# Performance work log

Measured on AMD Instinct MI355X. Metric: run time of the kernel, lower is better.

## Reference

```python
import jax, jax.numpy as jnp
import numpy as np
from jax import lax

N, IN_CH, OUT_CH, KERNEL, D = 16, 256, 256, 3, 4096
FACTOR = 2  # upsampling factor
RESAMPLE_K = (1.0, 3.0, 3.0, 1.0)


def _fir_kernel():
    # _setup_kernel: normalize to sum 1; upsample path scales by gain * factor
    k = np.asarray(RESAMPLE_K, dtype=np.float32)
    k = k / k.sum()
    return k * FACTOR  # gain = 1


def setup_inputs() -> dict:
    key = jax.random.key(0)
    k1, k2, k3 = jax.random.split(key, 3)
    x = jax.random.normal(k1, (N, IN_CH, D), dtype=jnp.float32)
    weight = jax.random.normal(k2, (OUT_CH, IN_CH, KERNEL), dtype=jnp.float32) * 0.05
    bias = jax.random.normal(k3, (OUT_CH,), dtype=jnp.float32) * 0.05
    return {"x": x, "weight": weight, "bias": bias}


def _upfirdn1d(x, k, pad0, pad1):
    # up=down=1 path of StyleGAN2 upfirdn1d: pad, then TRUE convolution with FIR k
    # (torch native impl flips k before F.conv1d). Depthwise via [N*C,1,L] reshape.
    n, c, _ = x.shape
    xp = jnp.pad(x, ((0, 0), (0, 0), (pad0, pad1)))
    kr = k[::-1][None, None, :]  # flip -> correlation == convolution
    y = lax.conv_general_dilated(
        xp.reshape(n * c, 1, -1), kr, window_strides=(1,), padding=[(0, 0)],
        dimension_numbers=("NCH", "OIH", "NCH"))
    return y.reshape(n, c, -1)


def _upsample_conv_1d(x, w):
    # torch: w reshaped/flipped/permuted then conv_transpose1d(stride=factor).
    # conv_transpose with that transformed weight == correlation with the ORIGINAL
    # w on an input dilated by `factor` with (convH-1) padding on both sides
    # (output_padding = 0 for these shapes).
    convH = w.shape[2]
    y = lax.conv_general_dilated(
        x, w, window_strides=(1,), padding=[(convH - 1, convH - 1)],
        lhs_dilation=(FACTOR,), dimension_numbers=("NCH", "OIH", "NCH"))
    k = jnp.asarray(_fir_kernel())
    p = k.shape[0] - FACTOR - (convH - 1)  # = 0 here
    pad0 = (p + 1) // 2 + FACTOR - 1
    pad1 = p // 2 + 1
    return _upfirdn1d(y, k, pad0, pad1)  # -> [N, C_out, D * FACTOR]


def reference(x, weight, bias):
    y = _upsample_conv_1d(x, weight)
    return y + bias[None, :, None]
```

## Files before the change

### kernel.cpp

```cpp
#include <hip/hip_runtime.h>
#include <hip/hip_bf16.h>

#define N_   16
#define CI_  256
#define CO_  256
#define D_   4096
#define DO_  8192
#define KTOT 768
#define XTROWS 4098
#define WT_ELEMS (512 * KTOT)
#define XT_ELEMS ((size_t)N_ * XTROWS * 256)

typedef short frag8 __attribute__((ext_vector_type(8)));
typedef float facc4 __attribute__((ext_vector_type(4)));

static __device__ __forceinline__ unsigned short f2bf(float f) {
    union { __hip_bfloat16 h; unsigned short u; } cv;
    cv.h = __float2bfloat16(f);
    return cv.u;
}

static __device__ __forceinline__ unsigned int pack2(float lo, float hi) {
    return (unsigned int)f2bf(lo) | ((unsigned int)f2bf(hi) << 16);
}

static __device__ __forceinline__ void async16(unsigned short* lds, const unsigned short* g) {
    __builtin_amdgcn_global_load_lds(
        (const __attribute__((address_space(1))) unsigned int*)g,
        (__attribute__((address_space(3))) unsigned int*)lds, 16, 0, 0);
}

__global__ __launch_bounds__(256) void prep_wt(const float* __restrict__ w,
                                               unsigned short* __restrict__ Wt) {
    const int ci = threadIdx.x;
    const int co = blockIdx.x;
    const float* wp = w + ((size_t)co * CI_ + ci) * 3;
    const float w0 = wp[0], w1 = wp[1], w2 = wp[2];
    const float e0 = 0.25f * w1 + 0.75f * w0;
    const float e1 = 0.75f * w2 + 0.75f * w1 + 0.25f * w0;
    const float e2 = 0.25f * w2;
    const float o0 = 0.25f * w0;
    const float o1 = 0.25f * w2 + 0.75f * w1 + 0.75f * w0;
    const float o2 = 0.75f * w2 + 0.25f * w1;
    unsigned short* pe = Wt + (size_t)(co * 2 + 0) * KTOT;
    unsigned short* po = Wt + (size_t)(co * 2 + 1) * KTOT;
    pe[0 * 256 + ci] = f2bf(e0); pe[1 * 256 + ci] = f2bf(e1); pe[2 * 256 + ci] = f2bf(e2);
    po[0 * 256 + ci] = f2bf(o0); po[1 * 256 + ci] = f2bf(o1); po[2 * 256 + ci] = f2bf(o2);
}

__global__ __launch_bounds__(256) void prep_xt2(const float* __restrict__ x,
                                                unsigned short* __restrict__ xt) {
    __shared__ unsigned int Lp[32][133];
    const int tid = threadIdx.x;
    const int t0  = blockIdx.x * 32;
    const int n   = blockIdx.y;
    const float* xn = x + (size_t)n * CI_ * D_;
    unsigned short* slab = xt + (size_t)n * XTROWS * 256;

    if (t0 == 0 && tid < 128)       ((unsigned int*)slab)[tid] = 0u;
    if (t0 == D_ - 32 && tid < 128) ((unsigned int*)(slab + (size_t)(XTROWS - 1) * 256))[tid] = 0u;

    const int cp_l  = tid >> 3;
    const int t_off = (tid & 7) * 4;

    #pragma unroll
    for (int p = 0; p < 4; ++p) {
        const int ci0 = p * 64 + cp_l * 2;
        float4 a = *(const float4*)(xn + (size_t)ci0 * D_ + t0 + t_off);
        float4 b = *(const float4*)(xn + (size_t)(ci0 + 1) * D_ + t0 + t_off);
        const int cp = p * 32 + cp_l;
        Lp[t_off + 0][cp] = pack2(a.x, b.x);
        Lp[t_off + 1][cp] = pack2(a.y, b.y);
        Lp[t_off + 2][cp] = pack2(a.z, b.z);
        Lp[t_off + 3][cp] = pack2(a.w, b.w);
    }
    __syncthreads();

    #pragma unroll
    for (int it = 0; it < 4; ++it) {
        const int row = it * 8 + (tid >> 5);
        const int c4  = (tid & 31) * 4;
        uint4 v;
        v.x = Lp[row][c4 + 0];
        v.y = Lp[row][c4 + 1];
        v.z = Lp[row][c4 + 2];
        v.w = Lp[row][c4 + 3];
        *(uint4*)(slab + (size_t)(1 + t0 + row) * 256 + c4 * 2) = v;
    }
}

__global__ __launch_bounds__(256) void gemm_upfir(
    const unsigned short* __restrict__ Wt, const unsigned short* __restrict__ xt,
    const float* __restrict__ bias, float* __restrict__ out)
{
    __shared__ __align__(16) unsigned short As[128 * 32];
    __shared__ __align__(16) unsigned short Bs[128 * 32];

    const int tid  = threadIdx.x;
    const int lane = tid & 63;
    const int wid  = tid >> 6;
    const int quad = lane >> 4;
    const int l16  = lane & 15;

    const int bt0 = blockIdx.x * 128;
    const int bm0 = blockIdx.y * 128;
    const int n   = blockIdx.z;

    const int srow = lane >> 2;
    const int slot = lane & 3;
    const unsigned short* gsrc;
    unsigned short* lbase;
    int ginc;
    if (wid < 2) {
        int row0 = wid * 64 + srow;
        int cg   = slot ^ ((row0 >> 1) & 3);
        gsrc  = Wt + (size_t)(bm0 + row0) * KTOT + cg * 8;
        lbase = As + wid * 2048;
        ginc  = 16 * KTOT;
    } else {
        int row0 = (wid - 2) * 64 + srow;
        int cg   = slot ^ ((row0 >> 1) & 3);
        gsrc  = xt + (size_t)n * XTROWS * 256 + (size_t)(bt0 + row0) * 256 + cg * 8;
        lbase = Bs + (wid - 2) * 2048;
        ginc  = 16 * 256;
    }

    const int swz = quad ^ ((l16 >> 1) & 3);
    const int wave_m = (wid & 1) * 64;
    const int wave_t = (wid >> 1) * 64;
    int aoff[4], boff[4];
    #pragma unroll
    for (int i = 0; i < 4; ++i) {
        aoff[i] = (wave_m + i * 16 + l16) * 32 + swz * 8;
        boff[i] = (wave_t + i * 16 + l16) * 32 + swz * 8;
    }

    facc4 acc[4][4] = {};

    for (int s = 0; s < 24; ++s) {
        #pragma unroll
        for (int i = 0; i < 4; ++i)
            async16(lbase + i * 512, gsrc + (size_t)i * ginc + s * 32);
        __syncthreads();
        frag8 af[4], bfr[4];
        #pragma unroll
        for (int i = 0; i < 4; ++i) af[i]  = *(const frag8*)(As + aoff[i]);
        #pragma unroll
        for (int i = 0; i < 4; ++i) bfr[i] = *(const frag8*)(Bs + boff[i]);
        #pragma unroll
        for (int mi = 0; mi < 4; ++mi)
            #pragma unroll
            for (int ti = 0; ti < 4; ++ti)
                acc[mi][ti] = __builtin_amdgcn_mfma_f32_16x16x32_bf16(
                    af[mi], bfr[ti], acc[mi][ti], 0, 0, 0);
        __syncthreads();
    }

    #pragma unroll
    for (int mi = 0; mi < 4; ++mi) {
        int m0  = bm0 + wave_m + mi * 16 + quad * 4;
        int co0 = m0 >> 1;
        float b0 = bias[co0];
        float b1 = bias[co0 + 1];
        #pragma unroll
        for (int ti = 0; ti < 4; ++ti) {
            int t = bt0 + wave_t + ti * 16 + l16;
            facc4 v = acc[mi][ti];
            float* p0 = out + ((size_t)(n * CO_ + co0)) * DO_ + 2 * t;
            float* p1 = p0 + DO_;
            *(float2*)p0 = make_float2(v.x + b0, v.y + b0);
            *(float2*)p1 = make_float2(v.z + b1, v.w + b1);
        }
    }
}

__global__ __launch_bounds__(256) void upconv_fir_f32(
    const float* __restrict__ x, const float* __restrict__ w,
    const float* __restrict__ bias, float* __restrict__ out)
{
    __shared__ float ws[CI_][4];
    const int tid = threadIdx.x;
    const int co  = blockIdx.y;
    const int n   = blockIdx.z;
    {
        const float* wc = w + (size_t)co * CI_ * 3;
        ws[tid][0] = wc[tid * 3 + 0];
        ws[tid][1] = wc[tid * 3 + 1];
        ws[tid][2] = wc[tid * 3 + 2];
        ws[tid][3] = 0.f;
    }
    __syncthreads();
    const int t0 = (blockIdx.x * 256 + tid) * 8;
    const float* xn = x + (size_t)n * CI_ * D_;
    float s[10], g[9];
    #pragma unroll
    for (int k = 0; k < 10; ++k) s[k] = 0.f;
    #pragma unroll
    for (int k = 0; k < 9; ++k) g[k] = 0.f;
    #pragma unroll 2
    for (int ci = 0; ci < CI_; ++ci) {
        const float* xr = xn + ci * D_;
        float4 va = *(const float4*)(xr + t0);
        float4 vb = *(const float4*)(xr + t0 + 4);
        float  xm = (t0 > 0)      ? xr[t0 - 1] : 0.f;
        float  xp = (t0 + 8 < D_) ? xr[t0 + 8] : 0.f;
        float4 wv = *(const float4*)(&ws[ci][0]);
        const float w0 = wv.x, w1 = wv.y, w2 = wv.z;
        float xa[10];
        xa[0] = xm; xa[1] = va.x; xa[2] = va.y; xa[3] = va.z; xa[4] = va.w;
        xa[5] = vb.x; xa[6] = vb.y; xa[7] = vb.z; xa[8] = vb.w; xa[9] = xp;
        #pragma unroll
        for (int k = 0; k < 10; ++k) s[k] += w1 * xa[k];
        #pragma unroll
        for (int k = 0; k < 9; ++k)  g[k] += w0 * xa[k] + w2 * xa[k + 1];
    }
    const float b = bias[co];
    float o16[16];
    #pragma unroll
    for (int tt = 0; tt < 8; ++tt) {
        o16[2 * tt]     = 0.25f * (s[tt] + g[tt + 1]) + 0.75f * (g[tt] + s[tt + 1]) + b;
        o16[2 * tt + 1] = 0.25f * (g[tt] + s[tt + 2]) + 0.75f * (s[tt + 1] + g[tt + 1]) + b;
    }
    float* ob = out + ((size_t)n * CO_ + co) * DO_ + 2 * t0;
    *(float4*)(ob + 0)  = make_float4(o16[0],  o16[1],  o16[2],  o16[3]);
    *(float4*)(ob + 4)  = make_float4(o16[4],  o16[5],  o16[6],  o16[7]);
    *(float4*)(ob + 8)  = make_float4(o16[8],  o16[9],  o16[10], o16[11]);
    *(float4*)(ob + 12) = make_float4(o16[12], o16[13], o16[14], o16[15]);
}

extern "C" void kernel_launch(void* const* d_in, const int* in_sizes, int n_in,
                              void* d_out, int out_size, void* d_ws, size_t ws_size,
                              hipStream_t stream) {
    const float* x  = (const float*)d_in[0];
    const float* w  = (const float*)d_in[1];
    const float* b  = (const float*)d_in[2];
    float* out      = (float*)d_out;

    const size_t need = (size_t)WT_ELEMS * 2 + XT_ELEMS * 2;
    if (ws_size >= need) {
        unsigned short* Wt = (unsigned short*)d_ws;
        unsigned short* xt = Wt + WT_ELEMS;
        prep_wt<<<dim3(CO_), 256, 0, stream>>>(w, Wt);
        prep_xt2<<<dim3(D_ / 32, N_), 256, 0, stream>>>(x, xt);
        gemm_upfir<<<dim3(D_ / 128, 4, N_), 256, 0, stream>>>(Wt, xt, b, out);
    } else {
        upconv_fir_f32<<<dim3(2, CO_, N_), 256, 0, stream>>>(x, w, b, out);
    }
}
```

Before: 246.4 us.

## Triple-buffer LDS tiles with async prefetch two stages ahead in GEMM loop

```diff
diff --git a/kernel.cpp b/kernel.cpp
--- a/kernel.cpp
+++ b/kernel.cpp
@@ -93,8 +93,8 @@
     const unsigned short* __restrict__ Wt, const unsigned short* __restrict__ xt,
     const float* __restrict__ bias, float* __restrict__ out)
 {
-    __shared__ __align__(16) unsigned short As[128 * 32];
-    __shared__ __align__(16) unsigned short Bs[128 * 32];
+    __shared__ __align__(16) unsigned short As[3][128 * 32];
+    __shared__ __align__(16) unsigned short Bs[3][128 * 32];
 
     const int tid  = threadIdx.x;
     const int lane = tid & 63;
@@ -109,20 +109,20 @@
     const int srow = lane >> 2;
     const int slot = lane & 3;
     const unsigned short* gsrc;
-    unsigned short* lbase;
+    int lds_off;
     int ginc;
     if (wid < 2) {
         int row0 = wid * 64 + srow;
         int cg   = slot ^ ((row0 >> 1) & 3);
-        gsrc  = Wt + (size_t)(bm0 + row0) * KTOT + cg * 8;
-        lbase = As + wid * 2048;
-        ginc  = 16 * KTOT;
+        gsrc    = Wt + (size_t)(bm0 + row0) * KTOT + cg * 8;
+        lds_off = wid * 2048;
+        ginc    = 16 * KTOT;
     } else {
         int row0 = (wid - 2) * 64 + srow;
         int cg   = slot ^ ((row0 >> 1) & 3);
-        gsrc  = xt + (size_t)n * XTROWS * 256 + (size_t)(bt0 + row0) * 256 + cg * 8;
-        lbase = Bs + (wid - 2) * 2048;
-        ginc  = 16 * 256;
+        gsrc    = xt + (size_t)n * XTROWS * 256 + (size_t)(bt0 + row0) * 256 + cg * 8;
+        lds_off = (wid - 2) * 2048;
+        ginc    = 16 * 256;
     }
 
     const int swz = quad ^ ((l16 >> 1) & 3);
@@ -137,23 +137,41 @@
 
     facc4 acc[4][4] = {};
 
+    {
+        unsigned short* s0 = (wid < 2 ? As[0] : Bs[0]) + lds_off;
+        unsigned short* s1 = (wid < 2 ? As[1] : Bs[1]) + lds_off;
+        #pragma unroll
+        for (int i = 0; i < 4; ++i) async16(s0 + i * 512, gsrc + (size_t)i * ginc);
+        #pragma unroll
+        for (int i = 0; i < 4; ++i) async16(s1 + i * 512, gsrc + (size_t)i * ginc + 32);
+    }
+
+    #pragma unroll
     for (int s = 0; s < 24; ++s) {
-        #pragma unroll
-        for (int i = 0; i < 4; ++i)
-            async16(lbase + i * 512, gsrc + (size_t)i * ginc + s * 32);
-        __syncthreads();
+        const int bc = s % 3;
+        const int bn = (s + 2) % 3;
+        if (s < 23) asm volatile("s_waitcnt vmcnt(4)" ::: "memory");
+        else        asm volatile("s_waitcnt vmcnt(0)" ::: "memory");
+        __builtin_amdgcn_s_barrier();
+        if (s + 2 < 24) {
+            unsigned short* sb = (wid < 2 ? As[bn] : Bs[bn]) + lds_off;
+            #pragma unroll
+            for (int i = 0; i < 4; ++i)
+                async16(sb + i * 512, gsrc + (size_t)i * ginc + (size_t)(s + 2) * 32);
+        }
+        const unsigned short* ab = As[bc];
+        const unsigned short* bb = Bs[bc];
         frag8 af[4], bfr[4];
         #pragma unroll
-        for (int i = 0; i < 4; ++i) af[i]  = *(const frag8*)(As + aoff[i]);
-        #pragma unroll
-        for (int i = 0; i < 4; ++i) bfr[i] = *(const frag8*)(Bs + boff[i]);
+        for (int i = 0; i < 4; ++i) af[i]  = *(const frag8*)(ab + aoff[i]);
+        #pragma unroll
+        for (int i = 0; i < 4; ++i) bfr[i] = *(const frag8*)(bb + boff[i]);
         #pragma unroll
         for (int mi = 0; mi < 4; ++mi)
             #pragma unroll
             for (int ti = 0; ti < 4; ++ti)
                 acc[mi][ti] = __builtin_amdgcn_mfma_f32_16x16x32_bf16(
                     af[mi], bfr[ti], acc[mi][ti], 0, 0, 0);
-        __syncthreads();
     }
 
     #pragma unroll
```

New measurement: 238.1 us. 1.03x faster.

## Rewrite GEMM as 256x256-tile, 8-wave, double-buffered pipelined MFMA kernel

Applied to the files above, without the earlier changes.

```diff
diff --git a/kernel.cpp b/kernel.cpp
--- a/kernel.cpp
+++ b/kernel.cpp
@@ -29,6 +29,9 @@
         (const __attribute__((address_space(1))) unsigned int*)g,
         (__attribute__((address_space(3))) unsigned int*)lds, 16, 0, 0);
 }
+
+#define DSR_(dst, addr, litstr) \
+    asm volatile("ds_read_b128 %0, %1 offset:" litstr : "=&v"(dst) : "v"(addr))
 
 __global__ __launch_bounds__(256) void prep_wt(const float* __restrict__ w,
                                                unsigned short* __restrict__ Wt) {
@@ -89,12 +92,11 @@
     }
 }
 
-__global__ __launch_bounds__(256) void gemm_upfir(
+__global__ __launch_bounds__(512, 2) void gemm_upfir8(
     const unsigned short* __restrict__ Wt, const unsigned short* __restrict__ xt,
     const float* __restrict__ bias, float* __restrict__ out)
 {
-    __shared__ __align__(16) unsigned short As[128 * 32];
-    __shared__ __align__(16) unsigned short Bs[128 * 32];
+    __shared__ __align__(16) unsigned short SL[65536];
 
     const int tid  = threadIdx.x;
     const int lane = tid & 63;
@@ -102,70 +104,121 @@
     const int quad = lane >> 4;
     const int l16  = lane & 15;
 
-    const int bt0 = blockIdx.x * 128;
-    const int bm0 = blockIdx.y * 128;
+    const int bt0 = blockIdx.x * 256;
+    const int bm0 = blockIdx.y * 256;
     const int n   = blockIdx.z;
 
-    const int srow = lane >> 2;
-    const int slot = lane & 3;
-    const unsigned short* gsrc;
-    unsigned short* lbase;
-    int ginc;
-    if (wid < 2) {
-        int row0 = wid * 64 + srow;
-        int cg   = slot ^ ((row0 >> 1) & 3);
-        gsrc  = Wt + (size_t)(bm0 + row0) * KTOT + cg * 8;
-        lbase = As + wid * 2048;
-        ginc  = 16 * KTOT;
-    } else {
-        int row0 = (wid - 2) * 64 + srow;
-        int cg   = slot ^ ((row0 >> 1) & 3);
-        gsrc  = xt + (size_t)n * XTROWS * 256 + (size_t)(bt0 + row0) * 256 + cg * 8;
-        lbase = Bs + (wid - 2) * 2048;
-        ginc  = 16 * 256;
-    }
+    const int srow = wid * 16 + (lane >> 2);
+    const int cg   = (lane & 3) ^ ((lane >> 3) & 3);
+    const unsigned short* sA = Wt + (size_t)(bm0 + srow) * KTOT + cg * 8;
+    const unsigned short* sB = xt + (size_t)n * XTROWS * 256
+                                  + (size_t)(bt0 + srow) * 256 + cg * 8;
+
+    #define STAGE_A(u, mh) do {                                                     \
+        async16(SL + (((u)&1)*16384 + (mh)*8192 + 0*4096 + wid*512),                \
+                sA + (size_t)(mh)*128*KTOT + (u)*64 + 0);                           \
+        async16(SL + (((u)&1)*16384 + (mh)*8192 + 1*4096 + wid*512),                \
+                sA + (size_t)(mh)*128*KTOT + (u)*64 + 32); } while (0)
+    #define STAGE_B(u, th) do {                                                     \
+        async16(SL + (32768 + ((u)&1)*16384 + (th)*8192 + 0*4096 + wid*512),        \
+                sB + (size_t)(th)*128*256 + (u)*64 + 0);                            \
+        async16(SL + (32768 + ((u)&1)*16384 + (th)*8192 + 1*4096 + wid*512),        \
+                sB + (size_t)(th)*128*256 + (u)*64 + 32); } while (0)
 
     const int swz = quad ^ ((l16 >> 1) & 3);
-    const int wave_m = (wid & 1) * 64;
-    const int wave_t = (wid >> 1) * 64;
-    int aoff[4], boff[4];
-    #pragma unroll
-    for (int i = 0; i < 4; ++i) {
-        aoff[i] = (wave_m + i * 16 + l16) * 32 + swz * 8;
-        boff[i] = (wave_t + i * 16 + l16) * 32 + swz * 8;
-    }
-
-    facc4 acc[4][4] = {};
-
-    for (int s = 0; s < 24; ++s) {
-        #pragma unroll
-        for (int i = 0; i < 4; ++i)
-            async16(lbase + i * 512, gsrc + (size_t)i * ginc + s * 32);
-        __syncthreads();
-        frag8 af[4], bfr[4];
-        #pragma unroll
-        for (int i = 0; i < 4; ++i) af[i]  = *(const frag8*)(As + aoff[i]);
-        #pragma unroll
-        for (int i = 0; i < 4; ++i) bfr[i] = *(const frag8*)(Bs + boff[i]);
-        #pragma unroll
-        for (int mi = 0; mi < 4; ++mi)
-            #pragma unroll
-            for (int ti = 0; ti < 4; ++ti)
-                acc[mi][ti] = __builtin_amdgcn_mfma_f32_16x16x32_bf16(
-                    af[mi], bfr[ti], acc[mi][ti], 0, 0, 0);
-        __syncthreads();
-    }
-
-    #pragma unroll
-    for (int mi = 0; mi < 4; ++mi) {
-        int m0  = bm0 + wave_m + mi * 16 + quad * 4;
+    const int mh  = wid & 1;
+    const int wm  = mh * 128;
+    const int wt  = ((wid >> 1) & 3) * 64;
+    const unsigned base = (unsigned)(size_t)&SL[0];
+    const unsigned aB = base + (unsigned)(mh * 16384 + l16 * 64 + swz * 16);
+    const unsigned bB = base + 65536u
+                      + (unsigned)(((wid >> 2) & 1) * 16384
+                                   + (((wid >> 1) & 1) * 64 + l16) * 64 + swz * 16);
+
+    facc4 acc[8][4] = {};
+
+    STAGE_A(0, 0); STAGE_A(0, 1); STAGE_B(0, 0); STAGE_B(0, 1);
+    STAGE_A(1, 0); STAGE_A(1, 1);
+    asm volatile("s_waitcnt vmcnt(4)" ::: "memory");
+    __builtin_amdgcn_s_barrier();
+
+    #define MM(m, t)                                                                 \
+        acc[m][t] = __builtin_amdgcn_mfma_f32_16x16x32_bf16(a[m][0], b[t][0], acc[m][t], 0, 0, 0); \
+        acc[m][t] = __builtin_amdgcn_mfma_f32_16x16x32_bf16(a[m][1], b[t][1], acc[m][t], 0, 0, 0);
+
+    #pragma unroll 2
+    for (int u = 0; u < 12; ++u) {
+        const unsigned au = aB + (unsigned)((u & 1) << 15);
+        const unsigned bu = bB + (unsigned)((u & 1) << 15);
+        frag8 a[8][2], b[4][2];
+
+        DSR_(a[0][0], au, "0");    DSR_(a[0][1], au, "8192");
+        DSR_(a[1][0], au, "1024"); DSR_(a[1][1], au, "9216");
+        DSR_(a[2][0], au, "2048"); DSR_(a[2][1], au, "10240");
+        DSR_(a[3][0], au, "3072"); DSR_(a[3][1], au, "11264");
+        DSR_(b[0][0], bu, "0");    DSR_(b[0][1], bu, "8192");
+        DSR_(b[1][0], bu, "1024"); DSR_(b[1][1], bu, "9216");
+        if (u < 11) STAGE_B(u + 1, 0);
+        __builtin_amdgcn_s_barrier();
+        asm volatile("s_waitcnt lgkmcnt(0)" ::: "memory");
+        __builtin_amdgcn_sched_barrier(0);
+        __builtin_amdgcn_s_setprio(1);
+        MM(0, 0) MM(1, 0) MM(2, 0) MM(3, 0)
+        MM(0, 1) MM(1, 1) MM(2, 1) MM(3, 1)
+        __builtin_amdgcn_s_setprio(0);
+        __builtin_amdgcn_s_barrier();
+
+        DSR_(a[4][0], au, "4096"); DSR_(a[4][1], au, "12288");
+        DSR_(a[5][0], au, "5120"); DSR_(a[5][1], au, "13312");
+        DSR_(a[6][0], au, "6144"); DSR_(a[6][1], au, "14336");
+        DSR_(a[7][0], au, "7168"); DSR_(a[7][1], au, "15360");
+        if (u < 11) STAGE_B(u + 1, 1);
+        __builtin_amdgcn_s_barrier();
+        asm volatile("s_waitcnt lgkmcnt(0)" ::: "memory");
+        __builtin_amdgcn_sched_barrier(0);
+        __builtin_amdgcn_s_setprio(1);
+        MM(4, 0) MM(5, 0) MM(6, 0) MM(7, 0)
+        MM(4, 1) MM(5, 1) MM(6, 1) MM(7, 1)
+        __builtin_amdgcn_s_setprio(0);
+        __builtin_amdgcn_s_barrier();
+
+        DSR_(b[2][0], bu, "2048"); DSR_(b[2][1], bu, "10240");
+        DSR_(b[3][0], bu, "3072"); DSR_(b[3][1], bu, "11264");
+        if (u < 10) STAGE_A(u + 2, 0);
+        __builtin_amdgcn_s_barrier();
+        asm volatile("s_waitcnt lgkmcnt(0)" ::: "memory");
+        __builtin_amdgcn_sched_barrier(0);
+        __builtin_amdgcn_s_setprio(1);
+        MM(4, 2) MM(5, 2) MM(6, 2) MM(7, 2)
+        MM(4, 3) MM(5, 3) MM(6, 3) MM(7, 3)
+        __builtin_amdgcn_s_setprio(0);
+        __builtin_amdgcn_s_barrier();
+
+        if (u < 10) STAGE_A(u + 2, 1);
+        __builtin_amdgcn_s_barrier();
+        __builtin_amdgcn_sched_barrier(0);
+        __builtin_amdgcn_s_setprio(1);
+        MM(0, 2) MM(1, 2) MM(2, 2) MM(3, 2)
+        MM(0, 3) MM(1, 3) MM(2, 3) MM(3, 3)
+        __builtin_amdgcn_s_setprio(0);
+        if (u < 10) { asm volatile("s_waitcnt vmcnt(4)" ::: "memory"); }
+        else        { asm volatile("s_waitcnt vmcnt(0)" ::: "memory"); }
+        __builtin_amdgcn_s_barrier();
+    }
+    #undef MM
+    #undef STAGE_A
+    #undef STAGE_B
+
+    #pragma unroll
+    for (int m8 = 0; m8 < 8; ++m8) {
+        int m0  = bm0 + wm + m8 * 16 + quad * 4;
         int co0 = m0 >> 1;
         float b0 = bias[co0];
         float b1 = bias[co0 + 1];
         #pragma unroll
-        for (int ti = 0; ti < 4; ++ti) {
-            int t = bt0 + wave_t + ti * 16 + l16;
-            facc4 v = acc[mi][ti];
+        for (int t4 = 0; t4 < 4; ++t4) {
+            int t = bt0 + wt + t4 * 16 + l16;
+            facc4 v = acc[m8][t4];
             float* p0 = out + ((size_t)(n * CO_ + co0)) * DO_ + 2 * t;
             float* p1 = p0 + DO_;
             *(float2*)p0 = make_float2(v.x + b0, v.y + b0);
@@ -242,7 +295,7 @@
         unsigned short* xt = Wt + WT_ELEMS;
         prep_wt<<<dim3(CO_), 256, 0, stream>>>(w, Wt);
         prep_xt2<<<dim3(D_ / 32, N_), 256, 0, stream>>>(x, xt);
-        gemm_upfir<<<dim3(D_ / 128, 4, N_), 256, 0, stream>>>(Wt, xt, b, out);
+        gemm_upfir8<<<dim3(D_ / 256, 2, N_), 512, 0, stream>>>(Wt, xt, b, out);
     } else {
         upconv_fir_f32<<<dim3(2, CO_, N_), 256, 0, stream>>>(x, w, b, out);
     }
```

New measurement: 236.1 us. 1.04x faster.
